# Optimization experiments

Hardware: AMD Instinct MI355X
Metric: run time of the kernel (lower is better)

The kernel has to match this reference:

```python
import jax, jax.numpy as jnp
import numpy as np


def setup_inputs() -> dict:
    key = jax.random.key(0)
    X = jax.random.normal(key, (4096, 32000), dtype=jnp.float32)
    return {"X": X}


def reference(X):
    # Sparsemax along last dim (dim=-1, k=None => full sort path).
    d = X.shape[-1]
    x = X - jnp.max(X, axis=-1, keepdims=True)
    # sort descending
    srt = -jnp.sort(-x, axis=-1)                       # [B, d]
    topk_cumsum = jnp.cumsum(srt, axis=-1) - 1.0       # [B, d]
    rho = jnp.arange(1, d + 1, dtype=x.dtype)          # [d]
    support = rho * srt > topk_cumsum                  # [B, d] bool
    supp_size = jnp.sum(support, axis=-1, keepdims=True)  # [B, 1] int
    tau = jnp.take_along_axis(topk_cumsum, supp_size - 1, axis=-1)
    tau = tau / supp_size.astype(x.dtype)
    return jnp.maximum(x - tau, 0.0)
```

## Files before the change

kernel.cpp:

```cpp
#include <hip/hip_runtime.h>
#include <float.h>


#define D     32000
#define D4    (D / 4)
#define CAP   2048
#define BLOCK 256

__global__ __launch_bounds__(BLOCK) void sparsemax_kernel(const float* __restrict__ X,
                                                          float* __restrict__ out) {
    const int row = blockIdx.x;
    const int tid = threadIdx.x;
    const size_t base = (size_t)row * D;
    const float4* __restrict__ x4 = (const float4*)(X + base);
    float4* __restrict__ o4 = (float4*)(out + base);

    float m = -FLT_MAX;
    for (int i = tid; i < D4; i += BLOCK) {
        float4 v = x4[i];
        m = fmaxf(m, fmaxf(fmaxf(v.x, v.y), fmaxf(v.z, v.w)));
    }
    #pragma unroll
    for (int off = 32; off > 0; off >>= 1)
        m = fmaxf(m, __shfl_down(m, off, 64));

    __shared__ float warpmax[BLOCK / 64];
    __shared__ float srowmax;
    __shared__ int scount;
    if ((tid & 63) == 0) warpmax[tid >> 6] = m;
    if (tid == 0) scount = 0;
    __syncthreads();
    if (tid == 0) {
        float mm = warpmax[0];
        #pragma unroll
        for (int w = 1; w < BLOCK / 64; ++w) mm = fmaxf(mm, warpmax[w]);
        srowmax = mm;
    }
    __syncthreads();
    const float rowmax = srowmax;
    const float thr = rowmax - 1.0f;

    __shared__ float cand[CAP];
    for (int i = tid; i < D4; i += BLOCK) {
        float4 v = x4[i];
        float a0 = v.x, a1 = v.y, a2 = v.z, a3 = v.w;
        if (a0 > thr) { int p = atomicAdd(&scount, 1); if (p < CAP) cand[p] = a0 - rowmax; }
        if (a1 > thr) { int p = atomicAdd(&scount, 1); if (p < CAP) cand[p] = a1 - rowmax; }
        if (a2 > thr) { int p = atomicAdd(&scount, 1); if (p < CAP) cand[p] = a2 - rowmax; }
        if (a3 > thr) { int p = atomicAdd(&scount, 1); if (p < CAP) cand[p] = a3 - rowmax; }
    }
    __syncthreads();
    int K = scount;
    if (K > CAP) K = CAP;

    __shared__ float sorted[CAP];
    for (int t = tid; t < K; t += BLOCK) {
        float v = cand[t];
        int rank = 0;
        for (int j = 0; j < K; ++j) {
            float u = cand[j];
            rank += (u > v) || (u == v && j < t);
        }
        sorted[rank] = v;
    }
    __syncthreads();

    __shared__ float stau;
    if (tid == 0) {
        float cs = 0.0f, cs_k = 0.0f;
        int k = 1;
        for (int j = 0; j < K; ++j) {
            cs += sorted[j];
            if ((float)(j + 1) * sorted[j] > cs - 1.0f) { k = j + 1; cs_k = cs; }
        }
        stau = (cs_k - 1.0f) / (float)k;
    }
    __syncthreads();
    const float sub = rowmax + stau;

    for (int i = tid; i < D4; i += BLOCK) {
        float4 v = x4[i];
        float4 r;
        r.x = fmaxf(v.x - sub, 0.0f);
        r.y = fmaxf(v.y - sub, 0.0f);
        r.z = fmaxf(v.z - sub, 0.0f);
        r.w = fmaxf(v.w - sub, 0.0f);
        o4[i] = r;
    }
}

extern "C" void kernel_launch(void* const* d_in, const int* in_sizes, int n_in,
                              void* d_out, int out_size, void* d_ws, size_t ws_size,
                              hipStream_t stream) {
    const float* X = (const float*)d_in[0];
    float* out = (float*)d_out;
    const int rows = in_sizes[0] / D;
    sparsemax_kernel<<<rows, BLOCK, 0, stream>>>(X, out);
}
```

Before: 960.0 us.

## Single-pass fused max and candidate collection with sparse output scatter

Merges the max pass and candidate-collection pass into one read of the row, using a running shared max estimate (atomicMax on order-preserving encoded floats) as a loose threshold. Candidates are stored with their indices, then filtered against the true max before the rank sort. The output is zero-filled during the same pass and only the positive support entries are scattered at the end, so the third full read of X is removed. This cuts global reads from three passes to one but adds more shared atomics early on, when the estimate is low and many elements pass it, and risks overflowing CAP when the estimate lags. It also relies on global write ordering within a thread for the zero-fill followed by the scatter.

```diff
diff --git a/kernel.cpp b/kernel.cpp
--- a/kernel.cpp
+++ b/kernel.cpp
@@ -4,8 +4,18 @@
 
 #define D     32000
 #define D4    (D / 4)
-#define CAP   2048
 #define BLOCK 256
+#define CAP   3072
+#define PCAP  512
+
+__device__ __forceinline__ unsigned enc_f32(float f) {
+    unsigned u = __float_as_uint(f);
+    return (u & 0x80000000u) ? ~u : (u | 0x80000000u);
+}
+__device__ __forceinline__ float dec_f32(unsigned k) {
+    unsigned u = (k & 0x80000000u) ? (k ^ 0x80000000u) : ~k;
+    return __uint_as_float(u);
+}
 
 __global__ __launch_bounds__(BLOCK) void sparsemax_kernel(const float* __restrict__ X,
                                                           float* __restrict__ out) {
@@ -15,77 +25,108 @@
     const float4* __restrict__ x4 = (const float4*)(X + base);
     float4* __restrict__ o4 = (float4*)(out + base);
 
-    float m = -FLT_MAX;
-    for (int i = tid; i < D4; i += BLOCK) {
+    __shared__ float    candV[CAP];
+    __shared__ int      candI[CAP];
+    __shared__ float    pv[PCAP];
+    __shared__ int      pidx[PCAP];
+    __shared__ float    ssorted[PCAP];
+    __shared__ unsigned smax_key;
+    __shared__ int      scount, scount2;
+    __shared__ float    swarp[BLOCK / 64];
+    __shared__ float    s_truemax, s_tau;
+
+    if (tid == 0) { smax_key = 0u; scount = 0; scount2 = 0; }
+    __syncthreads();
+
+    const float4 zero4 = make_float4(0.f, 0.f, 0.f, 0.f);
+
+    float4 v0 = x4[tid];
+    o4[tid] = zero4;
+    float tmax = fmaxf(fmaxf(v0.x, v0.y), fmaxf(v0.z, v0.w));
+    atomicMax(&smax_key, enc_f32(tmax));
+    __syncthreads();
+
+    {
+        float est = dec_f32(*(volatile unsigned*)&smax_key);
+        float thr = est - 1.0f;
+        int gi = tid * 4;
+        if (v0.x > thr) { int p = atomicAdd(&scount, 1); if (p < CAP) { candV[p] = v0.x; candI[p] = gi + 0; } }
+        if (v0.y > thr) { int p = atomicAdd(&scount, 1); if (p < CAP) { candV[p] = v0.y; candI[p] = gi + 1; } }
+        if (v0.z > thr) { int p = atomicAdd(&scount, 1); if (p < CAP) { candV[p] = v0.z; candI[p] = gi + 2; } }
+        if (v0.w > thr) { int p = atomicAdd(&scount, 1); if (p < CAP) { candV[p] = v0.w; candI[p] = gi + 3; } }
+    }
+
+    for (int i = tid + BLOCK; i < D4; i += BLOCK) {
+        float est = dec_f32(*(volatile unsigned*)&smax_key);
+        float thr = est - 1.0f;
         float4 v = x4[i];
-        m = fmaxf(m, fmaxf(fmaxf(v.x, v.y), fmaxf(v.z, v.w)));
+        o4[i] = zero4;
+        int gi = i * 4;
+        if (v.x > thr) { int p = atomicAdd(&scount, 1); if (p < CAP) { candV[p] = v.x; candI[p] = gi + 0; } }
+        if (v.y > thr) { int p = atomicAdd(&scount, 1); if (p < CAP) { candV[p] = v.y; candI[p] = gi + 1; } }
+        if (v.z > thr) { int p = atomicAdd(&scount, 1); if (p < CAP) { candV[p] = v.z; candI[p] = gi + 2; } }
+        if (v.w > thr) { int p = atomicAdd(&scount, 1); if (p < CAP) { candV[p] = v.w; candI[p] = gi + 3; } }
+        float m4 = fmaxf(fmaxf(v.x, v.y), fmaxf(v.z, v.w));
+        if (m4 > tmax) {
+            tmax = m4;
+            atomicMax(&smax_key, enc_f32(tmax));
+        }
     }
+    __syncthreads();
+
+    float m = tmax;
     #pragma unroll
     for (int off = 32; off > 0; off >>= 1)
         m = fmaxf(m, __shfl_down(m, off, 64));
-
-    __shared__ float warpmax[BLOCK / 64];
-    __shared__ float srowmax;
-    __shared__ int scount;
-    if ((tid & 63) == 0) warpmax[tid >> 6] = m;
-    if (tid == 0) scount = 0;
+    if ((tid & 63) == 0) swarp[tid >> 6] = m;
     __syncthreads();
     if (tid == 0) {
-        float mm = warpmax[0];
+        float mm = swarp[0];
         #pragma unroll
-        for (int w = 1; w < BLOCK / 64; ++w) mm = fmaxf(mm, warpmax[w]);
-        srowmax = mm;
+        for (int w = 1; w < BLOCK / 64; ++w) mm = fmaxf(mm, swarp[w]);
+        s_truemax = mm;
     }
     __syncthreads();
-    const float rowmax = srowmax;
-    const float thr = rowmax - 1.0f;
+    const float truemax = s_truemax;
 
-    __shared__ float cand[CAP];
-    for (int i = tid; i < D4; i += BLOCK) {
-        float4 v = x4[i];
-        float a0 = v.x, a1 = v.y, a2 = v.z, a3 = v.w;
-        if (a0 > thr) { int p = atomicAdd(&scount, 1); if (p < CAP) cand[p] = a0 - rowmax; }
-        if (a1 > thr) { int p = atomicAdd(&scount, 1); if (p < CAP) cand[p] = a1 - rowmax; }
-        if (a2 > thr) { int p = atomicAdd(&scount, 1); if (p < CAP) cand[p] = a2 - rowmax; }
-        if (a3 > thr) { int p = atomicAdd(&scount, 1); if (p < CAP) cand[p] = a3 - rowmax; }
+    int K = scount; if (K > CAP) K = CAP;
+    const float fthr = truemax - 1.0f;
+    for (int t = tid; t < K; t += BLOCK) {
+        float v = candV[t];
+        if (v > fthr) {
+            int p = atomicAdd(&scount2, 1);
+            if (p < PCAP) { pv[p] = v - truemax; pidx[p] = candI[t]; }
+        }
     }
     __syncthreads();
-    int K = scount;
-    if (K > CAP) K = CAP;
+    int K2 = scount2; if (K2 > PCAP) K2 = PCAP;
 
-    __shared__ float sorted[CAP];
-    for (int t = tid; t < K; t += BLOCK) {
-        float v = cand[t];
+    for (int t = tid; t < K2; t += BLOCK) {
+        float v = pv[t];
         int rank = 0;
-        for (int j = 0; j < K; ++j) {
-            float u = cand[j];
+        for (int j = 0; j < K2; ++j) {
+            float u = pv[j];
             rank += (u > v) || (u == v && j < t);
         }
-        sorted[rank] = v;
+        ssorted[rank] = v;
     }
     __syncthreads();
 
-    __shared__ float stau;
     if (tid == 0) {
         float cs = 0.0f, cs_k = 0.0f;
         int k = 1;
-        for (int j = 0; j < K; ++j) {
-            cs += sorted[j];
-            if ((float)(j + 1) * sorted[j] > cs - 1.0f) { k = j + 1; cs_k = cs; }
+        for (int j = 0; j < K2; ++j) {
+            cs += ssorted[j];
+            if ((float)(j + 1) * ssorted[j] > cs - 1.0f) { k = j + 1; cs_k = cs; }
         }
-        stau = (cs_k - 1.0f) / (float)k;
+        s_tau = (cs_k - 1.0f) / (float)k;
     }
     __syncthreads();
-    const float sub = rowmax + stau;
+    const float tau = s_tau;
 
-    for (int i = tid; i < D4; i += BLOCK) {
-        float4 v = x4[i];
-        float4 r;
-        r.x = fmaxf(v.x - sub, 0.0f);
-        r.y = fmaxf(v.y - sub, 0.0f);
-        r.z = fmaxf(v.z - sub, 0.0f);
-        r.w = fmaxf(v.w - sub, 0.0f);
-        o4[i] = r;
+    for (int t = tid; t < K2; t += BLOCK) {
+        float val = pv[t] - tau;
+        if (val > 0.0f) out[base + pidx[t]] = val;
     }
 }
 
```

Result: faster. 866.1 us (-9.8%).
